# Optimization experiments

Measured on AMD Instinct MI355X. Metric: run time of the kernel, lower is better.

## Reference

```python
import jax, jax.numpy as jnp
import numpy as np

B, DIM, H, W = 4, 192, 128, 128
HEADS = 4
K_RATES = (1.0 / 2, 2.0 / 3, 3.0 / 4, 4.0 / 5)


def setup_inputs() -> dict:
    key = jax.random.key(0)
    ks = jax.random.split(key, 5)
    x = jax.random.normal(ks[0], (B, DIM, H, W), jnp.float32)
    w_qkv = jax.random.normal(ks[1], (3 * DIM, DIM, 1, 1), jnp.float32) * 0.05
    w_dw = jax.random.normal(ks[2], (3 * DIM, 1, 3, 3), jnp.float32) * 0.05
    w_proj = jax.random.normal(ks[3], (DIM, DIM, 1, 1), jnp.float32) * 0.05
    temperature = jnp.ones((HEADS, 1, 1), jnp.float32)
    attn_w = jnp.full((4,), 0.2, jnp.float32)
    return {"x": x, "w_qkv": w_qkv, "w_dw": w_dw, "w_proj": w_proj,
            "temperature": temperature, "attn_w": attn_w}


def _conv1x1(x, w):
    # x: [b,c,h,w], w: [o,c,1,1]
    return jnp.einsum('bchw,oc->bohw', x, w[:, :, 0, 0])


def _dwconv3x3(x, w):
    # depthwise 3x3, padding=1; w: [c,1,3,3]
    return jax.lax.conv_general_dilated(
        x, w, window_strides=(1, 1), padding=((1, 1), (1, 1)),
        dimension_numbers=('NCHW', 'OIHW', 'NCHW'),
        feature_group_count=x.shape[1])


def _l2norm(x, eps=1e-12):
    # matches F.normalize(dim=-1): x / max(||x||, eps)
    n = jnp.sqrt(jnp.sum(x * x, axis=-1, keepdims=True))
    return x / jnp.maximum(n, eps)


def reference(x, w_qkv, w_dw, w_proj, temperature, attn_w):
    b, c, h, w = x.shape
    qkv = _dwconv3x3(_conv1x1(x, w_qkv), w_dw)  # [b, 3c, h, w]
    q, k, v = jnp.split(qkv, 3, axis=1)

    def heads(t):
        return t.reshape(b, HEADS, c // HEADS, h * w)  # [b, head, C, hw]

    q, k, v = heads(q), heads(k), heads(v)
    q = _l2norm(q)
    k = _l2norm(k)

    C = q.shape[2]
    attn = jnp.einsum('bhcn,bhdn->bhcd', q, k) * temperature[None]  # [b,head,C,C]

    out = jnp.zeros_like(v)
    for i, rate in enumerate(K_RATES):
        k_val = max(1, int(C * rate))
        _, idx = jax.lax.top_k(attn, k_val)  # [b,head,C,k]
        mask = jax.nn.one_hot(idx, C, dtype=attn.dtype).sum(axis=-2)  # [b,head,C,C]
        branch = jnp.where(mask > 0, attn, -jnp.inf)
        branch = jax.nn.softmax(branch, axis=-1)
        out = out + jnp.einsum('bhcd,bhdn->bhcn', branch, v) * attn_w[i]

    out = out.reshape(b, c, h, w)
    return _conv1x1(out, w_proj)
```

## Files before the change

kernel.cpp:

```cpp
#include <hip/hip_runtime.h>
#include <math.h>
#include <stdint.h>

#define BB 4
#define DIM 192
#define HEADS 4
#define CH 48
#define HW 16384
#define C3 576
#define NCHUNK 64

typedef unsigned short ushort_t;
typedef __attribute__((ext_vector_type(8))) short short8;
typedef __attribute__((ext_vector_type(4))) float floatx4;

__device__ __forceinline__ float bf2f(unsigned int u) {
    union { unsigned int i; float f; } v; v.i = u << 16; return v.f;
}
__device__ __forceinline__ ushort_t f2bf(float f) {
    union { float f; unsigned int i; } v; v.f = f;
    unsigned int x = v.i;
    x += 0x7fffu + ((x >> 16) & 1u);
    return (ushort_t)(x >> 16);
}

__global__ __launch_bounds__(256) void zero_init(float* __restrict__ p, int n) {
    int i = blockIdx.x * 256 + threadIdx.x;
    if (i < n) p[i] = 0.f;
}

__global__ __launch_bounds__(256) void convert_split(
    const float* __restrict__ in, ushort_t* __restrict__ hi,
    ushort_t* __restrict__ lo, int n)
{
    int i = blockIdx.x * 256 + threadIdx.x;
    if (i < n) {
        float f = in[i];
        ushort_t h = f2bf(f);
        hi[i] = h;
        lo[i] = f2bf(f - bf2f(h));
    }
}

__global__ __launch_bounds__(256) void tconv(
    const float* __restrict__ in, ushort_t* __restrict__ out_hi,
    ushort_t* __restrict__ out_lo, int wlo, long inStride)
{
    int z = blockIdx.z;
    in += (long)z * inStride;
    out_hi += (long)z * HW * DIM;
    if (wlo) out_lo += (long)z * HW * DIM;
    __shared__ ushort_t th[64][80];
    __shared__ ushort_t tl[64][80];
    int n0 = blockIdx.x * 64, k0 = blockIdx.y * 64;
    int t = threadIdx.x;
#pragma unroll
    for (int i = 0; i < 4; ++i) {
        int kl = (t >> 4) + 16 * i;
        float4 v = *(const float4*)(in + (long)(k0 + kl) * HW + n0 + (t & 15) * 4);
        int nl = (t & 15) * 4;
        ushort_t hx = f2bf(v.x), hy = f2bf(v.y), hz = f2bf(v.z), hw = f2bf(v.w);
        th[nl + 0][kl] = hx; th[nl + 1][kl] = hy;
        th[nl + 2][kl] = hz; th[nl + 3][kl] = hw;
        if (wlo) {
            tl[nl + 0][kl] = f2bf(v.x - bf2f(hx));
            tl[nl + 1][kl] = f2bf(v.y - bf2f(hy));
            tl[nl + 2][kl] = f2bf(v.z - bf2f(hz));
            tl[nl + 3][kl] = f2bf(v.w - bf2f(hw));
        }
    }
    __syncthreads();
#pragma unroll
    for (int i = 0; i < 2; ++i) {
        int nl = t >> 2, seg = (t & 3) + 4 * i;
        *(uint4*)(out_hi + (long)(n0 + nl) * DIM + k0 + seg * 8) = *(uint4*)&th[nl][seg * 8];
        if (wlo)
            *(uint4*)(out_lo + (long)(n0 + nl) * DIM + k0 + seg * 8) = *(uint4*)&tl[nl][seg * 8];
    }
}

#define BS_STRIDE 104
template<int TERMS>
__global__ __launch_bounds__(256) void gemm_reg(
    const ushort_t* __restrict__ Ahi, const ushort_t* __restrict__ Alo,
    const ushort_t* __restrict__ BThi, const ushort_t* __restrict__ BTlo,
    float* __restrict__ C, int M, int N,
    long strideA, long strideB, long strideC)
{
    int z = blockIdx.z;
    Ahi += z * strideA; Alo += z * strideA;
    BThi += z * strideB; BTlo += z * strideB;
    C += z * strideC;
    __shared__ ushort_t Bs0[128 * BS_STRIDE];
    __shared__ ushort_t Bs1[128 * BS_STRIDE];
    int t = threadIdx.x;
    int wave = t >> 6, lane = t & 63;
    int l15 = lane & 15, quad = lane >> 4;
    int m0 = blockIdx.y * 64, n0 = blockIdx.x * 128;
    int wm = (wave & 1) * 32, wn = (wave >> 1) * 64;
    floatx4 acc[2][4];
#pragma unroll
    for (int i = 0; i < 2; ++i)
#pragma unroll
        for (int j = 0; j < 4; ++j) acc[i][j] = (floatx4){0.f, 0.f, 0.f, 0.f};

    if (TERMS == 1) {
        short8 af[2][6];
#pragma unroll
        for (int mi = 0; mi < 2; ++mi)
#pragma unroll
            for (int k0 = 0; k0 < 6; ++k0)
                af[mi][k0] = *(const short8*)(Ahi
                    + (long)(m0 + wm + mi * 16 + l15) * 192 + k0 * 32 + quad * 8);
        for (int i = t; i < 3072; i += 256) {
            int r = i / 24, seg = i % 24;
            uint4 v = *(const uint4*)(BThi + (long)(n0 + r) * 192 + seg * 8);
            ushort_t* dst = (seg < 12) ? &Bs0[r * BS_STRIDE + seg * 8]
                                       : &Bs1[r * BS_STRIDE + (seg - 12) * 8];
            *(uint4*)dst = v;
        }
        __syncthreads();
#pragma unroll
        for (int k0 = 0; k0 < 6; ++k0) {
            int ks = k0 * 32 + quad * 8;
            const ushort_t* buf = (ks < 96) ? Bs0 : Bs1;
            int col = (ks < 96) ? ks : ks - 96;
            short8 bf[4];
#pragma unroll
            for (int ni = 0; ni < 4; ++ni)
                bf[ni] = *(const short8*)&buf[(wn + ni * 16 + l15) * BS_STRIDE + col];
#pragma unroll
            for (int mi = 0; mi < 2; ++mi)
#pragma unroll
                for (int ni = 0; ni < 4; ++ni)
                    acc[mi][ni] = __builtin_amdgcn_mfma_f32_16x16x32_bf16(
                        af[mi][k0], bf[ni], acc[mi][ni], 0, 0, 0);
        }
    } else {
#pragma unroll
        for (int kh = 0; kh < 2; ++kh) {
            short8 ah[2][3], al[2][3];
#pragma unroll
            for (int mi = 0; mi < 2; ++mi)
#pragma unroll
                for (int k0 = 0; k0 < 3; ++k0) {
                    long off = (long)(m0 + wm + mi * 16 + l15) * 192
                             + kh * 96 + k0 * 32 + quad * 8;
                    ah[mi][k0] = *(const short8*)(Ahi + off);
                    al[mi][k0] = *(const short8*)(Alo + off);
                }
            if (kh) __syncthreads();
            for (int i = t; i < 1536; i += 256) {
                int r = i / 12, seg = i % 12;
                long goff = (long)(n0 + r) * 192 + kh * 96 + seg * 8;
                *(uint4*)&Bs0[r * BS_STRIDE + seg * 8] = *(const uint4*)(BThi + goff);
                *(uint4*)&Bs1[r * BS_STRIDE + seg * 8] = *(const uint4*)(BTlo + goff);
            }
            __syncthreads();
#pragma unroll
            for (int k0 = 0; k0 < 3; ++k0) {
                int col = k0 * 32 + quad * 8;
                short8 bh[4], bl[4];
#pragma unroll
                for (int ni = 0; ni < 4; ++ni) {
                    bh[ni] = *(const short8*)&Bs0[(wn + ni * 16 + l15) * BS_STRIDE + col];
                    bl[ni] = *(const short8*)&Bs1[(wn + ni * 16 + l15) * BS_STRIDE + col];
                }
#pragma unroll
                for (int mi = 0; mi < 2; ++mi)
#pragma unroll
                    for (int ni = 0; ni < 4; ++ni) {
                        acc[mi][ni] = __builtin_amdgcn_mfma_f32_16x16x32_bf16(
                            ah[mi][k0], bh[ni], acc[mi][ni], 0, 0, 0);
                        acc[mi][ni] = __builtin_amdgcn_mfma_f32_16x16x32_bf16(
                            ah[mi][k0], bl[ni], acc[mi][ni], 0, 0, 0);
                        acc[mi][ni] = __builtin_amdgcn_mfma_f32_16x16x32_bf16(
                            al[mi][k0], bh[ni], acc[mi][ni], 0, 0, 0);
                    }
            }
        }
    }
#pragma unroll
    for (int mi = 0; mi < 2; ++mi)
#pragma unroll
        for (int ni = 0; ni < 4; ++ni) {
            long base = (long)(m0 + wm + mi * 16 + quad * 4) * N + n0 + wn + ni * 16 + l15;
#pragma unroll
            for (int r = 0; r < 4; ++r)
                C[base + (long)r * N] = acc[mi][ni][r];
        }
}

__global__ __launch_bounds__(256) void dwconv3x3_lds(
    const float* __restrict__ in, const float* __restrict__ w,
    float* __restrict__ out, float* __restrict__ normsq,
    int c0, int chunk)
{
    __shared__ float tile[10][132];
    int z = blockIdx.z;
    int cl = blockIdx.y;
    int gc = c0 + cl;
    in  += (long)z * chunk * HW + (long)cl * HW;
    out += (long)z * C3 * HW + (long)gc * HW;
    int y0 = blockIdx.x * 8;
    const float* wc = w + gc * 9;
    float wf[9];
#pragma unroll
    for (int i = 0; i < 9; ++i) wf[i] = wc[i];
    int t = threadIdx.x;
    if (t < 10) { tile[t][0] = 0.f; tile[t][129] = 0.f; }
    for (int i = t; i < 320; i += 256) {
        int r = i >> 5, c4 = (i & 31) * 4;
        int gy = y0 - 1 + r;
        float4 v = {0.f, 0.f, 0.f, 0.f};
        if (gy >= 0 && gy < 128) v = *(const float4*)(in + gy * 128 + c4);
        tile[r][1 + c4] = v.x; tile[r][2 + c4] = v.y;
        tile[r][3 + c4] = v.z; tile[r][4 + c4] = v.w;
    }
    __syncthreads();
    int yl = t >> 5, xl = (t & 31) * 4;
    float s0 = 0.f, s1 = 0.f, s2 = 0.f, s3 = 0.f;
#pragma unroll
    for (int r = 0; r < 3; ++r) {
        float c0v = tile[yl + r][xl + 0], c1v = tile[yl + r][xl + 1];
        float c2v = tile[yl + r][xl + 2], c3v = tile[yl + r][xl + 3];
        float c4v = tile[yl + r][xl + 4], c5v = tile[yl + r][xl + 5];
        float w0 = wf[r * 3], w1 = wf[r * 3 + 1], w2 = wf[r * 3 + 2];
        s0 += w0 * c0v + w1 * c1v + w2 * c2v;
        s1 += w0 * c1v + w1 * c2v + w2 * c3v;
        s2 += w0 * c2v + w1 * c3v + w2 * c4v;
        s3 += w0 * c3v + w1 * c4v + w2 * c5v;
    }
    float4 o = {s0, s1, s2, s3};
    *(float4*)(out + (y0 + yl) * 128 + xl) = o;
    if (gc < 2 * DIM) {
        __syncthreads();
        float* red = (float*)tile;
        red[t] = s0 * s0 + s1 * s1 + s2 * s2 + s3 * s3;
        __syncthreads();
        for (int off = 128; off > 0; off >>= 1) {
            if (t < off) red[t] += red[t + off];
            __syncthreads();
        }
        if (t == 0) atomicAdd(&normsq[z * 512 + gc], red[0]);
    }
}

__global__ __launch_bounds__(256) void attn_partial2(
    const float* __restrict__ dw, float* __restrict__ partial)
{
    int z = blockIdx.z, h = blockIdx.y, pidx = blockIdx.x;
    int n0 = pidx * (HW / NCHUNK);
    dw += (long)z * C3 * HW;
    __shared__ float qs[48][68];
    __shared__ float ks[48][68];
    const float* qb = dw + (long)(h * CH) * HW + n0;
    const float* kb = dw + (long)(DIM + h * CH) * HW + n0;
    int t = threadIdx.x;
    int tx = t & 15, ty = t >> 4;
    int c0 = ty * 3, d0 = tx * 3;
    float acc[3][3] = {};
#pragma unroll
    for (int rnd = 0; rnd < 4; ++rnd) {
        if (rnd) __syncthreads();
#pragma unroll
        for (int i = 0; i < 3; ++i) {
            int f = t + i * 256;
            int row = f >> 4, c4 = (f & 15) * 4;
            float4 qv = *(const float4*)(qb + (long)row * HW + rnd * 64 + c4);
            float4 kv = *(const float4*)(kb + (long)row * HW + rnd * 64 + c4);
            *(float4*)&qs[row][c4] = qv;
            *(float4*)&ks[row][c4] = kv;
        }
        __syncthreads();
        for (int nv = 0; nv < 16; ++nv) {
            float4 qa[3], kb4[3];
#pragma unroll
            for (int i = 0; i < 3; ++i) qa[i] = *(const float4*)&qs[c0 + i][nv * 4];
#pragma unroll
            for (int j = 0; j < 3; ++j) kb4[j] = *(const float4*)&ks[d0 + j][nv * 4];
#pragma unroll
            for (int i = 0; i < 3; ++i)
#pragma unroll
                for (int j = 0; j < 3; ++j)
                    acc[i][j] += qa[i].x * kb4[j].x + qa[i].y * kb4[j].y
                               + qa[i].z * kb4[j].z + qa[i].w * kb4[j].w;
        }
    }
    float* pp = partial + ((long)(pidx * 16 + z * HEADS + h)) * 2304;
#pragma unroll
    for (int i = 0; i < 3; ++i)
#pragma unroll
        for (int j = 0; j < 3; ++j)
            pp[(c0 + i) * CH + d0 + j] = acc[i][j];
}

__global__ __launch_bounds__(256) void topk_combine2(
    const float* __restrict__ partial, const float* __restrict__ normsq,
    const float* __restrict__ temp, const float* __restrict__ attn_w,
    float* __restrict__ Wc)
{
    int z = blockIdx.y;
    int wave = threadIdx.x >> 6, lane = threadIdx.x & 63;
    int rid = blockIdx.x * 4 + wave;
    int c = rid % CH, h = rid / CH;
    int d = lane;
    float a = -INFINITY;
    if (d < 48) {
        float s = 0.f;
        const float* pp = partial + (long)(z * HEADS + h) * 2304 + c * CH + d;
        for (int p = 0; p < NCHUNK; ++p) s += pp[(long)p * 16 * 2304];
        float invq = 1.0f / fmaxf(sqrtf(normsq[z * 512 + h * CH + c]), 1e-12f);
        float invk = 1.0f / fmaxf(sqrtf(normsq[z * 512 + DIM + h * CH + d]), 1e-12f);
        a = s * invq * invk * temp[h];
    }
    float m = a;
#pragma unroll
    for (int off = 32; off > 0; off >>= 1) m = fmaxf(m, __shfl_xor(m, off, 64));
    float e = (d < 48) ? expf(a - m) : 0.f;
    int rank = 0;
    for (int j = 0; j < 48; ++j) {
        float aj = __shfl(a, j, 64);
        rank += (aj > a) || (aj == a && j < d);
    }
    const int kv[4] = {24, 32, 36, 38};
    float s = 0.f;
#pragma unroll
    for (int i = 0; i < 4; ++i) {
        float contrib = (d < 48 && rank < kv[i]) ? e : 0.f;
#pragma unroll
        for (int off = 32; off > 0; off >>= 1) contrib += __shfl_xor(contrib, off, 64);
        s += (rank < kv[i]) ? attn_w[i] / contrib : 0.f;
    }
    if (d < 48) Wc[(long)z * 9216 + (long)rid * CH + d] = e * s;
}

__global__ __launch_bounds__(256) void build_m(
    const float* __restrict__ wproj, const float* __restrict__ Wc,
    ushort_t* __restrict__ Mb)
{
    int z = blockIdx.y;
    int idx = blockIdx.x * 256 + threadIdx.x;
    if (idx >= DIM * DIM) return;
    int cg = idx % DIM;
    int o  = idx / DIM;
    int h = cg / CH, d = cg % CH;
    const float* wp = wproj + o * DIM + h * CH;
    const float* wcc = Wc + (long)z * 9216 + (long)h * CH * CH + d;
    float s = 0.f;
#pragma unroll
    for (int ch = 0; ch < CH; ++ch) s += wp[ch] * wcc[ch * CH];
    Mb[(long)z * DIM * DIM + idx] = f2bf(s);
}

extern "C" void kernel_launch(void* const* d_in, const int* in_sizes, int n_in,
                              void* d_out, int out_size, void* d_ws, size_t ws_size,
                              hipStream_t stream) {
    const float* x      = (const float*)d_in[0];
    const float* w_qkv  = (const float*)d_in[1];
    const float* w_dw   = (const float*)d_in[2];
    const float* w_proj = (const float*)d_in[3];
    const float* temper = (const float*)d_in[4];
    const float* attn_w = (const float*)d_in[5];
    float* out = (float*)d_out;

    char* p = (char*)d_ws;
    float* dw        = (float*)p;      p += (long)BB * C3 * HW * 4;
    ushort_t* xT_hi  = (ushort_t*)p;   p += (long)BB * HW * DIM * 2;
    ushort_t* xT_lo  = (ushort_t*)p;   p += (long)BB * HW * DIM * 2;
    ushort_t* wq_hi  = (ushort_t*)p;   p += (long)C3 * DIM * 2;
    ushort_t* wq_lo  = (ushort_t*)p;   p += (long)C3 * DIM * 2;
    float* normsq    = (float*)p;      p += (long)BB * 512 * 4;
    float* partial   = (float*)p;      p += (long)NCHUNK * 16 * 2304 * 4;
    float* Wc        = (float*)p;      p += (long)BB * 9216 * 4;
    ushort_t* Mb     = (ushort_t*)p;   p += (long)BB * DIM * DIM * 2;
    float* pre       = (float*)p;
    long avail = (long)ws_size - (long)(p - (char*)d_ws);
    int chunk = 64;
    if (avail >= (long)BB * 192 * HW * 4) chunk = 192;

    zero_init<<<(BB * 512 + 255) / 256, 256, 0, stream>>>(normsq, BB * 512);
    convert_split<<<(C3 * DIM + 255) / 256, 256, 0, stream>>>(
        w_qkv, wq_hi, wq_lo, C3 * DIM);
    tconv<<<dim3(HW / 64, DIM / 64, BB), 256, 0, stream>>>(
        x, xT_hi, xT_lo, 1, (long)DIM * HW);

    for (int c0 = 0; c0 < C3; c0 += chunk) {
        if (c0 < 2 * DIM)
            gemm_reg<3><<<dim3(HW / 128, chunk / 64, BB), 256, 0, stream>>>(
                wq_hi + (long)c0 * DIM, wq_lo + (long)c0 * DIM, xT_hi, xT_lo,
                pre, chunk, HW, 0L, (long)HW * DIM, (long)chunk * HW);
        else
            gemm_reg<1><<<dim3(HW / 128, chunk / 64, BB), 256, 0, stream>>>(
                wq_hi + (long)c0 * DIM, wq_hi + (long)c0 * DIM, xT_hi, xT_hi,
                pre, chunk, HW, 0L, (long)HW * DIM, (long)chunk * HW);
        dwconv3x3_lds<<<dim3(16, chunk, BB), 256, 0, stream>>>(
            pre, w_dw, dw, normsq, c0, chunk);
    }
    attn_partial2<<<dim3(NCHUNK, HEADS, BB), 256, 0, stream>>>(dw, partial);
    topk_combine2<<<dim3(48, BB), 256, 0, stream>>>(
        partial, normsq, temper, attn_w, Wc);
    build_m<<<dim3((DIM * DIM + 255) / 256, BB), 256, 0, stream>>>(w_proj, Wc, Mb);
    tconv<<<dim3(HW / 64, DIM / 64, BB), 256, 0, stream>>>(
        dw + (long)2 * DIM * HW, xT_hi, xT_lo, 0, (long)C3 * HW);
    gemm_reg<1><<<dim3(HW / 128, DIM / 64, BB), 256, 0, stream>>>(
        Mb, Mb, xT_hi, xT_hi, out, DIM, HW,
        (long)DIM * DIM, (long)HW * DIM, (long)DIM * HW);
}
```

Measured before the change: 391.4 us.

## Store q/k as split bf16 and compute Gram partials with MFMA

The depthwise conv now writes q and k as hi/lo bf16 pairs and v as fp32 into a separate buffer. The q·k^T partial Gram kernel is rewritten to use bf16 MFMA with three-term split precision, reading operands straight from global memory, and reduces the per-wave results through LDS. This replaces the scalar fp32 LDS-tiled dot products and keeps roughly fp32 accuracy. The partial buffer now aliases the pre-conv scratch, which is safe only because that scratch is dead by the time the partials are written.

Measured after the change: 381.8 us. 2.5% less time.

```diff
diff --git a/kernel.cpp b/kernel.cpp
--- a/kernel.cpp
+++ b/kernel.cpp
@@ -193,7 +193,8 @@
 
 __global__ __launch_bounds__(256) void dwconv3x3_lds(
     const float* __restrict__ in, const float* __restrict__ w,
-    float* __restrict__ out, float* __restrict__ normsq,
+    ushort_t* __restrict__ qk_hi, ushort_t* __restrict__ qk_lo,
+    float* __restrict__ vbuf, float* __restrict__ normsq,
     int c0, int chunk)
 {
     __shared__ float tile[10][132];
@@ -201,7 +202,6 @@
     int cl = blockIdx.y;
     int gc = c0 + cl;
     in  += (long)z * chunk * HW + (long)cl * HW;
-    out += (long)z * C3 * HW + (long)gc * HW;
     int y0 = blockIdx.x * 8;
     const float* wc = w + gc * 9;
     float wf[9];
@@ -231,9 +231,19 @@
         s2 += w0 * c2v + w1 * c3v + w2 * c4v;
         s3 += w0 * c3v + w1 * c4v + w2 * c5v;
     }
-    float4 o = {s0, s1, s2, s3};
-    *(float4*)(out + (y0 + yl) * 128 + xl) = o;
+    long pix = (long)(y0 + yl) * 128 + xl;
     if (gc < 2 * DIM) {
+        ushort_t h0 = f2bf(s0), h1 = f2bf(s1), h2 = f2bf(s2), h3 = f2bf(s3);
+        ushort_t l0 = f2bf(s0 - bf2f(h0)), l1 = f2bf(s1 - bf2f(h1));
+        ushort_t l2 = f2bf(s2 - bf2f(h2)), l3 = f2bf(s3 - bf2f(h3));
+        uint2 ph, pl;
+        ph.x = (unsigned)h0 | ((unsigned)h1 << 16);
+        ph.y = (unsigned)h2 | ((unsigned)h3 << 16);
+        pl.x = (unsigned)l0 | ((unsigned)l1 << 16);
+        pl.y = (unsigned)l2 | ((unsigned)l3 << 16);
+        long rbase = ((long)z * 384 + gc) * HW + pix;
+        *(uint2*)(qk_hi + rbase) = ph;
+        *(uint2*)(qk_lo + rbase) = pl;
         __syncthreads();
         float* red = (float*)tile;
         red[t] = s0 * s0 + s1 * s1 + s2 * s2 + s3 * s3;
@@ -243,56 +253,85 @@
             __syncthreads();
         }
         if (t == 0) atomicAdd(&normsq[z * 512 + gc], red[0]);
-    }
-}
-
-__global__ __launch_bounds__(256) void attn_partial2(
-    const float* __restrict__ dw, float* __restrict__ partial)
+    } else {
+        float4 o = {s0, s1, s2, s3};
+        *(float4*)(vbuf + ((long)z * DIM + (gc - 2 * DIM)) * HW + pix) = o;
+    }
+}
+
+__global__ __launch_bounds__(256) void attn_mfma(
+    const ushort_t* __restrict__ qk_hi, const ushort_t* __restrict__ qk_lo,
+    float* __restrict__ partial)
 {
     int z = blockIdx.z, h = blockIdx.y, pidx = blockIdx.x;
-    int n0 = pidx * (HW / NCHUNK);
-    dw += (long)z * C3 * HW;
-    __shared__ float qs[48][68];
-    __shared__ float ks[48][68];
-    const float* qb = dw + (long)(h * CH) * HW + n0;
-    const float* kb = dw + (long)(DIM + h * CH) * HW + n0;
     int t = threadIdx.x;
-    int tx = t & 15, ty = t >> 4;
-    int c0 = ty * 3, d0 = tx * 3;
-    float acc[3][3] = {};
-#pragma unroll
-    for (int rnd = 0; rnd < 4; ++rnd) {
-        if (rnd) __syncthreads();
+    int wave = t >> 6, lane = t & 63;
+    int l15 = lane & 15, quad = lane >> 4;
+    long base = (long)z * 384 * HW;
+    const ushort_t* qh = qk_hi + base + (long)(h * CH) * HW;
+    const ushort_t* ql = qk_lo + base + (long)(h * CH) * HW;
+    const ushort_t* kh = qk_hi + base + (long)(DIM + h * CH) * HW;
+    const ushort_t* kl = qk_lo + base + (long)(DIM + h * CH) * HW;
+    int ncol0 = pidx * 256 + wave * 64;
+
+    floatx4 acc[3][3];
+#pragma unroll
+    for (int i = 0; i < 3; ++i)
+#pragma unroll
+        for (int j = 0; j < 3; ++j) acc[i][j] = (floatx4){0.f, 0.f, 0.f, 0.f};
+
+#pragma unroll
+    for (int ks = 0; ks < 2; ++ks) {
+        int col = ncol0 + ks * 32 + quad * 8;
+        short8 ah[3], al[3], bh[3], bl[3];
 #pragma unroll
         for (int i = 0; i < 3; ++i) {
-            int f = t + i * 256;
-            int row = f >> 4, c4 = (f & 15) * 4;
-            float4 qv = *(const float4*)(qb + (long)row * HW + rnd * 64 + c4);
-            float4 kv = *(const float4*)(kb + (long)row * HW + rnd * 64 + c4);
-            *(float4*)&qs[row][c4] = qv;
-            *(float4*)&ks[row][c4] = kv;
-        }
-        __syncthreads();
-        for (int nv = 0; nv < 16; ++nv) {
-            float4 qa[3], kb4[3];
-#pragma unroll
-            for (int i = 0; i < 3; ++i) qa[i] = *(const float4*)&qs[c0 + i][nv * 4];
-#pragma unroll
-            for (int j = 0; j < 3; ++j) kb4[j] = *(const float4*)&ks[d0 + j][nv * 4];
-#pragma unroll
-            for (int i = 0; i < 3; ++i)
-#pragma unroll
-                for (int j = 0; j < 3; ++j)
-                    acc[i][j] += qa[i].x * kb4[j].x + qa[i].y * kb4[j].y
-                               + qa[i].z * kb4[j].z + qa[i].w * kb4[j].w;
-        }
-    }
+            long ro = (long)(i * 16 + l15) * HW + col;
+            ah[i] = *(const short8*)(qh + ro);
+            al[i] = *(const short8*)(ql + ro);
+            bh[i] = *(const short8*)(kh + ro);
+            bl[i] = *(const short8*)(kl + ro);
+        }
+#pragma unroll
+        for (int mi = 0; mi < 3; ++mi)
+#pragma unroll
+            for (int ni = 0; ni < 3; ++ni) {
+                acc[mi][ni] = __builtin_amdgcn_mfma_f32_16x16x32_bf16(
+                    ah[mi], bh[ni], acc[mi][ni], 0, 0, 0);
+                acc[mi][ni] = __builtin_amdgcn_mfma_f32_16x16x32_bf16(
+                    ah[mi], bl[ni], acc[mi][ni], 0, 0, 0);
+                acc[mi][ni] = __builtin_amdgcn_mfma_f32_16x16x32_bf16(
+                    al[mi], bh[ni], acc[mi][ni], 0, 0, 0);
+            }
+    }
+
+    __shared__ float sred[2][48 * 50];
+    float* sb = sred[wave & 1];
+    if (wave < 2) {
+#pragma unroll
+        for (int mi = 0; mi < 3; ++mi)
+#pragma unroll
+            for (int ni = 0; ni < 3; ++ni)
+#pragma unroll
+                for (int r = 0; r < 4; ++r)
+                    sb[(mi * 16 + quad * 4 + r) * 50 + ni * 16 + l15] = acc[mi][ni][r];
+    }
+    __syncthreads();
+    if (wave >= 2) {
+#pragma unroll
+        for (int mi = 0; mi < 3; ++mi)
+#pragma unroll
+            for (int ni = 0; ni < 3; ++ni)
+#pragma unroll
+                for (int r = 0; r < 4; ++r)
+                    sb[(mi * 16 + quad * 4 + r) * 50 + ni * 16 + l15] += acc[mi][ni][r];
+    }
+    __syncthreads();
     float* pp = partial + ((long)(pidx * 16 + z * HEADS + h)) * 2304;
-#pragma unroll
-    for (int i = 0; i < 3; ++i)
-#pragma unroll
-        for (int j = 0; j < 3; ++j)
-            pp[(c0 + i) * CH + d0 + j] = acc[i][j];
+    for (int i = t; i < 2304; i += 256) {
+        int row = i / 48, colo = i - row * 48;
+        pp[i] = sred[0][row * 50 + colo] + sred[1][row * 50 + colo];
+    }
 }
 
 __global__ __launch_bounds__(256) void topk_combine2(
@@ -365,16 +404,18 @@
     float* out = (float*)d_out;
 
     char* p = (char*)d_ws;
-    float* dw        = (float*)p;      p += (long)BB * C3 * HW * 4;
+    ushort_t* qk_hi  = (ushort_t*)p;   p += (long)BB * 384 * HW * 2;
+    ushort_t* qk_lo  = (ushort_t*)p;   p += (long)BB * 384 * HW * 2;
+    float* vbuf      = (float*)p;      p += (long)BB * DIM * HW * 4;
     ushort_t* xT_hi  = (ushort_t*)p;   p += (long)BB * HW * DIM * 2;
     ushort_t* xT_lo  = (ushort_t*)p;   p += (long)BB * HW * DIM * 2;
     ushort_t* wq_hi  = (ushort_t*)p;   p += (long)C3 * DIM * 2;
     ushort_t* wq_lo  = (ushort_t*)p;   p += (long)C3 * DIM * 2;
     float* normsq    = (float*)p;      p += (long)BB * 512 * 4;
-    float* partial   = (float*)p;      p += (long)NCHUNK * 16 * 2304 * 4;
     float* Wc        = (float*)p;      p += (long)BB * 9216 * 4;
     ushort_t* Mb     = (ushort_t*)p;   p += (long)BB * DIM * DIM * 2;
     float* pre       = (float*)p;
+    float* partial   = pre;
     long avail = (long)ws_size - (long)(p - (char*)d_ws);
     int chunk = 64;
     if (avail >= (long)BB * 192 * HW * 4) chunk = 192;
@@ -395,14 +436,14 @@
                 wq_hi + (long)c0 * DIM, wq_hi + (long)c0 * DIM, xT_hi, xT_hi,
                 pre, chunk, HW, 0L, (long)HW * DIM, (long)chunk * HW);
         dwconv3x3_lds<<<dim3(16, chunk, BB), 256, 0, stream>>>(
-            pre, w_dw, dw, normsq, c0, chunk);
-    }
-    attn_partial2<<<dim3(NCHUNK, HEADS, BB), 256, 0, stream>>>(dw, partial);
+            pre, w_dw, qk_hi, qk_lo, vbuf, normsq, c0, chunk);
+    }
+    attn_mfma<<<dim3(NCHUNK, HEADS, BB), 256, 0, stream>>>(qk_hi, qk_lo, partial);
     topk_combine2<<<dim3(48, BB), 256, 0, stream>>>(
         partial, normsq, temper, attn_w, Wc);
     build_m<<<dim3((DIM * DIM + 255) / 256, BB), 256, 0, stream>>>(w_proj, Wc, Mb);
     tconv<<<dim3(HW / 64, DIM / 64, BB), 256, 0, stream>>>(
-        dw + (long)2 * DIM * HW, xT_hi, xT_lo, 0, (long)C3 * HW);
+        vbuf, xT_hi, xT_lo, 0, (long)DIM * HW);
     gemm_reg<1><<<dim3(HW / 128, DIM / 64, BB), 256, 0, stream>>>(
         Mb, Mb, xT_hi, xT_hi, out, DIM, HW,
         (long)DIM * DIM, (long)HW * DIM, (long)DIM * HW);
```
